# Kernel tuning notes

Measured on AMD Instinct MI355X. Metric: run time of the kernel, lower is better.

## Reference

```python
import jax, jax.numpy as jnp
import numpy as np

VOCAB, DIM, NC, KS, NCLASS = 50000, 300, 256, 3, 3
B, L1, L2 = 128, 512, 32
PAD = (KS - 1) // 2


def setup_inputs() -> dict:
    key = jax.random.key(0)
    ks = jax.random.split(key, 12)
    return {
        "context_ids": jax.random.randint(ks[0], (B, L1), 0, VOCAB),
        "context_masks": jnp.ones((B, L1), jnp.float32),
        "aspect_ids": jax.random.randint(ks[1], (B, L2), 0, VOCAB),
        "aspect_masks": jnp.ones((B, L2), jnp.float32),
        "wordmat": jax.random.normal(ks[2], (VOCAB, DIM), jnp.float32) * 0.1,
        "W": jax.random.normal(ks[3], (DIM, DIM), jnp.float32) * (2.0 / DIM) ** 0.5,
        "ctx_w": jax.random.normal(ks[4], (NC, DIM, KS), jnp.float32) * 0.02,
        "ctx_b": jnp.zeros((NC,), jnp.float32),
        "gate_w": jax.random.normal(ks[5], (NC, 2 * DIM, KS), jnp.float32) * 0.02,
        "gate_b": jnp.zeros((NC,), jnp.float32),
        "lin_w": jax.random.normal(ks[6], (NCLASS, NC), jnp.float32) * 0.05,
        "lin_b": jnp.zeros((NCLASS,), jnp.float32),
    }


def masked_softmax(A, mask):
    # A: (b, l1, l2); mask: (b, l2); normalize over dim=1 (l1), faithful to source
    A_max = jnp.max(A, axis=1, keepdims=True)
    A_exp = jnp.exp(A - A_max) * mask[:, None, :]
    return A_exp / (jnp.sum(A_exp, axis=1, keepdims=True) + 1e-10)


def conv1d(x, w, b):
    # x: (B, C_in, L), w: (C_out, C_in, K) -> (B, C_out, L)
    y = jax.lax.conv_general_dilated(x, w, (1,), [(PAD, PAD)],
                                     dimension_numbers=("NCH", "OIH", "NCH"))
    return y + b[None, :, None]


def reference(context_ids, context_masks, aspect_ids, aspect_masks,
              wordmat, W, ctx_w, ctx_b, gate_w, gate_b, lin_w, lin_b):
    context = wordmat[context_ids]          # (B, L1, D)
    aspect = wordmat[aspect_ids]            # (B, L2, D)
    # FullyAwareAttention
    sx = jax.nn.relu(jnp.einsum("bld,de->ble", context, W))
    sy = jax.nn.relu(jnp.einsum("bld,de->ble", aspect, W))
    s = jnp.einsum("bie,bje->bij", sx, sy)  # (B, L1, L2)
    alpha = masked_softmax(s, aspect_masks)
    att = jnp.einsum("bij,bjd->bid", alpha, aspect)  # (B, L1, D)
    gate_input = jnp.concatenate([context, att], axis=-1)  # (B, L1, 2D)
    sentiment = jnp.tanh(conv1d(context.transpose(0, 2, 1), ctx_w, ctx_b))
    gate = jax.nn.relu(conv1d(gate_input.transpose(0, 2, 1), gate_w, gate_b))
    out = jnp.max(sentiment * gate, axis=2)  # global maxpool over length
    return out @ lin_w.T + lin_b
```

## Files before the change

kernel.cpp:

```cpp
#include <hip/hip_runtime.h>
#include <hip/hip_bf16.h>
#include <math.h>
#include <stdint.h>

#define DIM 300
#define NC 256
#define KS 3
#define NCLASS 3
#define BB 128
#define L1 512
#define L2 32

#define XW 352
#define XROWS 514
#define ROW_B (XW * 2)
#define NKC 11
#define WP2_ELEMS (2 * 4 * 10 * 3 * 4 * 64 * 8)
#define WB_ELEMS (10 * 19 * 64 * 8)
#define WG2_ELEMS (3 * 10 * 16 * 64 * 8)
#define GT_ELEMS (BB * 3 * 32 * 256)
#define GATH_ELEMS (BB * L2 * 320)
#define WAVE_WP_B (10 * 3 * 4 * 1024)

#define ABUF_B 4224
#define EP_LD 516

typedef __attribute__((ext_vector_type(8))) short bf16x8;
typedef __attribute__((ext_vector_type(4))) short bf16x4;
typedef __attribute__((ext_vector_type(4))) float f32x4;

#define GLOBAL_AS __attribute__((address_space(1)))
#define LDS_AS __attribute__((address_space(3)))

__device__ __forceinline__ void gload_lds16(const void* g, void* l) {
    __builtin_amdgcn_global_load_lds((const GLOBAL_AS void*)g, (LDS_AS void*)l, 16, 0, 0);
}

static __device__ __forceinline__ short bfr(float x) {
    __hip_bfloat16 h = __float2bfloat16(x);
    return *(short*)&h;
}

__global__ void prep_all(const float* __restrict__ ctx_w,
                         const float* __restrict__ gate_w,
                         const float* __restrict__ Wm,
                         const int* __restrict__ aids,
                         const float* __restrict__ wordmat,
                         __hip_bfloat16* __restrict__ Wp2,
                         __hip_bfloat16* __restrict__ Wb,
                         __hip_bfloat16* __restrict__ Wg2,
                         __hip_bfloat16* __restrict__ aspb,
                         __hip_bfloat16* __restrict__ syb) {
    int idx = blockIdx.x * 256 + threadIdx.x;
    if (idx < WP2_ELEMS) {
        int jj = idx & 7;
        int lane = (idx >> 3) & 63;
        int n = (idx >> 9) & 3;
        int rest = idx >> 11;
        int tap = rest % 3;
        int r2 = rest / 3;
        int kc = r2 % 10;
        int w = r2 / 10;
        int role = w & 3, cbv = w >> 2;
        int k = kc * 32 + ((lane >> 4) << 3) + jj;
        int nl = role * 64 + n * 16 + (lane & 15);
        float v = 0.f;
        if (nl < 128) {
            int ch = cbv * 128 + nl;
            if (k < 300) v = ctx_w[(ch * DIM + k) * KS + tap];
        } else {
            int ch = cbv * 128 + (nl - 128);
            if (k < 300) v = gate_w[(ch * 2 * DIM + k) * KS + tap];
        }
        Wp2[idx] = __float2bfloat16(v);
        return;
    }
    idx -= WP2_ELEMS;
    if (idx < WB_ELEMS) {
        int j = idx & 7;
        int l = (idx >> 3) & 63;
        int r = idx >> 9;
        int nf = r % 19, kc = r / 19;
        int k = kc * 32 + ((l >> 4) << 3) + j;
        int n = nf * 16 + (l & 15);
        float v = (k < 300 && n < 300) ? Wm[k * DIM + n] : 0.f;
        Wb[idx] = __float2bfloat16(v);
        return;
    }
    idx -= WB_ELEMS;
    if (idx < WG2_ELEMS) {
        int jj = idx & 7;
        int lane = (idx >> 3) & 63;
        int rest = idx >> 9;
        int nf = rest % 16;
        int r2 = rest / 16;
        int kc = r2 % 10, tap = r2 / 10;
        int k = kc * 32 + ((lane >> 4) << 3) + jj;
        int n = nf * 16 + (lane & 15);
        float v = (k < 300) ? gate_w[(n * 2 * DIM + DIM + k) * KS + tap] : 0.f;
        Wg2[idx] = __float2bfloat16(v);
        return;
    }
    idx -= WG2_ELEMS;
    if (idx < GATH_ELEMS) {
        int row = idx / 320, d = idx - row * 320;
        if (d < DIM) {
            aspb[(size_t)row * 320 + d] = __float2bfloat16(wordmat[(size_t)aids[row] * DIM + d]);
        } else {
            aspb[(size_t)row * 320 + d] = __float2bfloat16(0.f);
            if (d >= 304) syb[(size_t)row * 320 + d] = __float2bfloat16(0.f);
        }
    }
}

__global__ __launch_bounds__(256) void xcat_x(const int* __restrict__ cids,
                                              const float* __restrict__ wordmat,
                                              __hip_bfloat16* __restrict__ Xc) {
    int t = threadIdx.x;
    int rloc = t >> 5, lane = t & 31;
    int row = blockIdx.x * 8 + rloc;
    int b = row >> 9, l = row & 511;
    size_t id = (size_t)cids[row];
    const float4* src = (const float4*)(wordmat + id * DIM);
    __hip_bfloat16* dst = Xc + ((size_t)b * XROWS + 1 + l) * XW;
    #pragma unroll
    for (int c = lane; c < 80; c += 32) {
        bf16x4 o;
        if (c < 75) {
            float4 f = src[c];
            o[0] = bfr(f.x); o[1] = bfr(f.y); o[2] = bfr(f.z); o[3] = bfr(f.w);
        } else {
            o = (bf16x4)0;
        }
        ((bf16x4*)dst)[c] = o;
    }
    if (blockIdx.x < 256 && t < 88) {
        int b2 = blockIdx.x >> 1;
        int gr = (blockIdx.x & 1) ? (XROWS - 1) : 0;
        ((bf16x4*)(Xc + ((size_t)b2 * XROWS + gr) * XW))[t] = (bf16x4)0;
    }
}

__global__ __launch_bounds__(256, 2) void asp_mfma(
        const __hip_bfloat16* __restrict__ aspb,
        const __hip_bfloat16* __restrict__ Wb,
        const __hip_bfloat16* __restrict__ Wg2,
        __hip_bfloat16* __restrict__ syb,
        __hip_bfloat16* __restrict__ Gt) {
    const int t = threadIdx.x, wave = t >> 6, l = t & 63;
    const int lane15 = l & 15, lq = l >> 4;
    if (blockIdx.x < 64) {
        const int g = blockIdx.x * 64 + wave * 16 + lane15;
        f32x4 acc[19];
        #pragma unroll
        for (int nf = 0; nf < 19; ++nf) acc[nf] = (f32x4)0.f;
        const bf16x8* Arow = (const bf16x8*)((const char*)aspb + (size_t)g * 640);
        const bf16x8* WbV = (const bf16x8*)Wb;
        for (int kc = 0; kc < 10; ++kc) {
            bf16x8 af = Arow[kc * 4 + lq];
            #pragma unroll
            for (int nf = 0; nf < 19; ++nf)
                acc[nf] = __builtin_amdgcn_mfma_f32_16x16x32_bf16(
                    af, WbV[(kc * 19 + nf) * 64 + l], acc[nf], 0, 0, 0);
        }
        #pragma unroll
        for (int nf = 0; nf < 19; ++nf) {
            int col = nf * 16 + lane15;
            #pragma unroll
            for (int i2 = 0; i2 < 4; ++i2) {
                int row = blockIdx.x * 64 + wave * 16 + lq * 4 + i2;
                syb[(size_t)row * 320 + col] = __float2bfloat16(fmaxf(acc[nf][i2], 0.f));
            }
        }
    } else {
        const int i = blockIdx.x - 64;
        const int b = i / 3, tap = i - b * 3;
        f32x4 acc[2][4];
        #pragma unroll
        for (int m = 0; m < 2; ++m)
            #pragma unroll
            for (int ni = 0; ni < 4; ++ni) acc[m][ni] = (f32x4)0.f;
        const char* Ab = (const char*)aspb + (size_t)b * 32 * 640;
        const bf16x8* WgV = (const bf16x8*)Wg2;
        for (int kc = 0; kc < 10; ++kc) {
            bf16x8 af[2];
            #pragma unroll
            for (int m = 0; m < 2; ++m)
                af[m] = *(const bf16x8*)(Ab + (size_t)(m * 16 + lane15) * 640 + kc * 64 + lq * 16);
            #pragma unroll
            for (int ni = 0; ni < 4; ++ni) {
                bf16x8 bw = WgV[((size_t)(tap * 10 + kc) * 16 + wave * 4 + ni) * 64 + l];
                #pragma unroll
                for (int m = 0; m < 2; ++m)
                    acc[m][ni] = __builtin_amdgcn_mfma_f32_16x16x32_bf16(af[m], bw, acc[m][ni], 0, 0, 0);
            }
        }
        #pragma unroll
        for (int m = 0; m < 2; ++m)
            #pragma unroll
            for (int ni = 0; ni < 4; ++ni) {
                int c = (wave * 4 + ni) * 16 + lane15;
                #pragma unroll
                for (int i2 = 0; i2 < 4; ++i2) {
                    int j = m * 16 + lq * 4 + i2;
                    Gt[((size_t)(b * 3 + tap) * 32 + j) * 256 + c] = __float2bfloat16(acc[m][ni][i2]);
                }
            }
    }
}

__global__ __launch_bounds__(256, 2) void sxs_mfma(
        const __hip_bfloat16* __restrict__ Xc,
        const __hip_bfloat16* __restrict__ Wb,
        const __hip_bfloat16* __restrict__ syb,
        float* __restrict__ s) {
    __shared__ __align__(16) char sxL[4 * 16 * 640];
    const int t = threadIdx.x, wave = t >> 6, l = t & 63;
    const int lane15 = l & 15, lq = l >> 4;
    const int lb = blockIdx.x, b = blockIdx.y;
    const int g = b * XROWS + 1 + lb * 64 + wave * 16 + lane15;

    f32x4 acc[19];
    #pragma unroll
    for (int nf = 0; nf < 19; ++nf) acc[nf] = (f32x4)0.f;

    const bf16x8* Arow = (const bf16x8*)((const char*)Xc + (size_t)g * ROW_B);
    const bf16x8* WbV = (const bf16x8*)Wb;
    for (int kc = 0; kc < 10; ++kc) {
        bf16x8 af = Arow[kc * 4 + lq];
        #pragma unroll
        for (int nf = 0; nf < 19; ++nf)
            acc[nf] = __builtin_amdgcn_mfma_f32_16x16x32_bf16(
                af, WbV[(kc * 19 + nf) * 64 + l], acc[nf], 0, 0, 0);
    }

    char* sxW = sxL + wave * (16 * 640);
    if (l < 32) {
        int row = l >> 1;
        int phys = (2 + (l & 1)) ^ ((row >> 2) & 3);
        *(f32x4*)(sxW + row * 640 + 576 + phys * 16) = (f32x4)0.f;
    }
    #pragma unroll
    for (int nf = 0; nf < 19; ++nf) {
        int col = nf * 16 + lane15;
        #pragma unroll
        for (int i2 = 0; i2 < 4; ++i2) {
            int row = lq * 4 + i2;
            int off = row * 640 + ((col >> 5) << 6) +
                      ((((col >> 3) & 3) ^ ((row >> 2) & 3)) << 4) + ((col & 7) << 1);
            *(__hip_bfloat16*)(sxW + off) = __float2bfloat16(fmaxf(acc[nf][i2], 0.f));
        }
    }
    f32x4 acc2[2];
    acc2[0] = (f32x4)0.f;
    acc2[1] = (f32x4)0.f;
    const bf16x8* syV = (const bf16x8*)syb + (size_t)b * 32 * 40;
    for (int kc = 0; kc < 10; ++kc) {
        bf16x8 af2 = *(const bf16x8*)(sxW + lane15 * 640 + kc * 64 +
                                      ((lq ^ ((lane15 >> 2) & 3)) << 4));
        #pragma unroll
        for (int nj = 0; nj < 2; ++nj) {
            bf16x8 bfj = syV[(nj * 16 + lane15) * 40 + kc * 4 + lq];
            acc2[nj] = __builtin_amdgcn_mfma_f32_16x16x32_bf16(af2, bfj, acc2[nj], 0, 0, 0);
        }
    }
    #pragma unroll
    for (int nj = 0; nj < 2; ++nj)
        #pragma unroll
        for (int i2 = 0; i2 < 4; ++i2) {
            int i = lb * 64 + wave * 16 + lq * 4 + i2;
            s[((size_t)b * L1 + i) * L2 + nj * 16 + lane15] = acc2[nj][i2];
        }
}

__global__ __launch_bounds__(256) void softmax_col(const float* __restrict__ s,
                                                   const float* __restrict__ amask,
                                                   __hip_bfloat16* __restrict__ Xc) {
    __shared__ float red[256];
    __shared__ float cmax[8], cscale[8];
    int b = blockIdx.x, jh = blockIdx.y, t = threadIdx.x;
    int jl = t & 7, j = jh * 8 + jl, ii = t >> 3;
    const float* sb = s + (size_t)b * L1 * L2;
    float v[16];
    float m = -1e30f;
    #pragma unroll
    for (int q = 0; q < 16; ++q) {
        v[q] = sb[(size_t)(ii + q * 32) * L2 + j];
        m = fmaxf(m, v[q]);
    }
    red[t] = m;
    __syncthreads();
    if (t < 8) {
        float mm = red[t];
        for (int p = 1; p < 32; ++p) mm = fmaxf(mm, red[p * 8 + t]);
        cmax[t] = mm;
    }
    __syncthreads();
    float cm = cmax[jl];
    float sum = 0.f;
    #pragma unroll
    for (int q = 0; q < 16; ++q) {
        v[q] = expf(v[q] - cm);
        sum += v[q];
    }
    red[t] = sum;
    __syncthreads();
    if (t < 8) {
        float ss = 0.f;
        for (int p = 0; p < 32; ++p) ss += red[p * 8 + t];
        float mk = amask[b * L2 + jh * 8 + t];
        cscale[t] = mk / (mk * ss + 1e-10f);
    }
    __syncthreads();
    float sc = cscale[jl];
    #pragma unroll
    for (int q = 0; q < 16; ++q) {
        int row = ii + q * 32;
        Xc[((size_t)b * XROWS + 1 + row) * XW + 320 + j] = __float2bfloat16(v[q] * sc);
    }
}

__global__ __launch_bounds__(512, 4) void conv_mfma(
        const __hip_bfloat16* __restrict__ Xc,
        const __hip_bfloat16* __restrict__ Wp2,
        const __hip_bfloat16* __restrict__ Gt,
        const float* __restrict__ ctx_b,
        const float* __restrict__ gate_b,
        float* __restrict__ part) {
    __shared__ __align__(16) char lds[16 * EP_LD * 4];
    const int t = threadIdx.x, wave = t >> 6, lane = t & 63;
    const int lane15 = lane & 15, lq = lane >> 4;
    const int lb = blockIdx.x, b = blockIdx.y, l0 = lb * 64;
    const bool isGate = wave >= 4;
    const int u = isGate ? wave - 4 : wave;
    const int cbv = u >> 1;
    const int role = isGate ? 2 + (u & 1) : (u & 1);

    f32x4 acc[4][4];
    #pragma unroll
    for (int m = 0; m < 4; ++m)
        #pragma unroll
        for (int n = 0; n < 4; ++n) acc[m][n] = (f32x4)0.f;

    const char* XcB = (const char*)Xc + ((size_t)b * XROWS + l0) * ROW_B;
    const char* bbase = (const char*)Wp2 + (size_t)(cbv * 4 + role) * WAVE_WP_B + lane * 16;

    #define STAGE_A(kc_, buf_) do {                                              \
        char* Ab_ = lds + (buf_) * ABUF_B;                                       \
        int chunk = wave * 64 + lane;                                            \
        if (chunk < 264) {                                                       \
            int row_ = chunk >> 2, c_ = chunk & 3;                               \
            int sc_ = (c_ ^ ((row_ >> 1) & 3)) << 4;                             \
            gload_lds16(XcB + (size_t)row_ * ROW_B + (kc_) * 64 + sc_,           \
                        Ab_ + wave * 1024);                                      \
        }                                                                        \
    } while (0)

    STAGE_A(0, 0);
    __syncthreads();

    for (int kc = 0; kc < NKC; ++kc) {
        const int cbuf = kc & 1;
        if (kc < NKC - 1) STAGE_A(kc + 1, cbuf ^ 1);
        const char* Ab = lds + cbuf * ABUF_B;
        if (kc < 10) {
            #pragma unroll
            for (int tap = 0; tap < 3; ++tap) {
                bf16x8 bw[4];
                #pragma unroll
                for (int n = 0; n < 4; ++n)
                    bw[n] = *(const bf16x8*)(bbase + (size_t)((kc * 3 + tap) * 4 + n) * 1024);
                bf16x8 af[4];
                #pragma unroll
                for (int m = 0; m < 4; ++m) {
                    int row = m * 16 + lane15 + tap;
                    af[m] = *(const bf16x8*)(Ab + row * 64 + ((lq ^ ((row >> 1) & 3)) << 4));
                }
                #pragma unroll
                for (int m = 0; m < 4; ++m)
                    #pragma unroll
                    for (int n = 0; n < 4; ++n)
                        acc[m][n] = __builtin_amdgcn_mfma_f32_16x16x32_bf16(
                            af[m], bw[n], acc[m][n], 0, 0, 0);
            }
        } else if (isGate) {
            const char* GtB = (const char*)Gt + (size_t)b * 3 * (32 * 256 * 2);
            #pragma unroll
            for (int tap = 0; tap < 3; ++tap) {
                bf16x8 bw[4];
                #pragma unroll
                for (int n = 0; n < 4; ++n) {
                    #pragma unroll
                    for (int jj = 0; jj < 8; ++jj)
                        ((short*)&bw[n])[jj] = *(const short*)(GtB +
                            (size_t)tap * (32 * 256 * 2) +
                            (size_t)(lq * 8 + jj) * 512 +
                            (size_t)(u * 64 + n * 16 + lane15) * 2);
                }
                bf16x8 af[4];
                #pragma unroll
                for (int m = 0; m < 4; ++m) {
                    int row = m * 16 + lane15 + tap;
                    af[m] = *(const bf16x8*)(Ab + row * 64 + ((lq ^ ((row >> 1) & 3)) << 4));
                }
                #pragma unroll
                for (int m = 0; m < 4; ++m)
                    #pragma unroll
                    for (int n = 0; n < 4; ++n)
                        acc[m][n] = __builtin_amdgcn_mfma_f32_16x16x32_bf16(
                            af[m], bw[n], acc[m][n], 0, 0, 0);
            }
        }
        __syncthreads();
    }
    #undef STAGE_A

    const int cl = t & 255, rh = t >> 8;
    const float bs = ctx_b[cl];
    const float bg = gate_b[cl];
    const int colbase = (isGate ? 256 + u * 64 : u * 64);
    float* ep = (float*)lds;
    float pm = -1e30f;
    for (int ms = 0; ms < 4; ++ms) {
        __syncthreads();
        #pragma unroll
        for (int n = 0; n < 4; ++n) {
            int col = colbase + (n << 4) + lane15;
            #pragma unroll
            for (int i2 = 0; i2 < 4; ++i2)
                ep[(lq * 4 + i2) * EP_LD + col] = acc[ms][n][i2];
        }
        __syncthreads();
        #pragma unroll
        for (int rr = 0; rr < 8; ++rr) {
            int r = rh * 8 + rr;
            float sv = ep[r * EP_LD + cl] + bs;
            float gv = ep[r * EP_LD + 256 + cl] + bg;
            pm = fmaxf(pm, tanhf(sv) * fmaxf(gv, 0.f));
        }
    }
    __syncthreads();
    ep[t] = pm;
    __syncthreads();
    if (t < 256)
        part[((size_t)b * 8 + lb) * 256 + t] = fmaxf(ep[t], ep[t + 256]);
}

__global__ __launch_bounds__(256) void finalize(const float* __restrict__ part,
                                                const float* __restrict__ lin_w,
                                                const float* __restrict__ lin_b,
                                                float* __restrict__ out) {
    __shared__ float pl[256];
    __shared__ float red[256];
    int b = blockIdx.x, t = threadIdx.x;
    float p = part[((size_t)b * 8) * 256 + t];
    for (int lb = 1; lb < 8; ++lb)
        p = fmaxf(p, part[((size_t)b * 8 + lb) * 256 + t]);
    pl[t] = p;
    __syncthreads();
    for (int n = 0; n < NCLASS; ++n) {
        red[t] = pl[t] * lin_w[n * NC + t];
        __syncthreads();
        for (int sft = 128; sft > 0; sft >>= 1) {
            if (t < sft) red[t] += red[t + sft];
            __syncthreads();
        }
        if (t == 0) out[b * NCLASS + n] = red[0] + lin_b[n];
        __syncthreads();
    }
}

extern "C" void kernel_launch(void* const* d_in, const int* in_sizes, int n_in,
                              void* d_out, int out_size, void* d_ws, size_t ws_size,
                              hipStream_t stream) {
    const int* cids = (const int*)d_in[0];
    const int* aids = (const int*)d_in[2];
    const float* amask = (const float*)d_in[3];
    const float* wordmat = (const float*)d_in[4];
    const float* Wm = (const float*)d_in[5];
    const float* ctx_w = (const float*)d_in[6];
    const float* ctx_b = (const float*)d_in[7];
    const float* gate_w = (const float*)d_in[8];
    const float* gate_b = (const float*)d_in[9];
    const float* lin_w = (const float*)d_in[10];
    const float* lin_b = (const float*)d_in[11];
    float* out = (float*)d_out;

    float* sbuf = (float*)d_ws;
    float* part = sbuf + 2097152;
    __hip_bfloat16* aspb = (__hip_bfloat16*)(part + 262144);
    __hip_bfloat16* sybf = aspb + 1310720;
    __hip_bfloat16* Wb   = sybf + 1310720;
    __hip_bfloat16* Wp2  = Wb + WB_ELEMS;
    __hip_bfloat16* Wg2  = Wp2 + WP2_ELEMS;
    __hip_bfloat16* Gt   = Wg2 + WG2_ELEMS;
    __hip_bfloat16* Xc   = Gt + GT_ELEMS;

    const int prepN = WP2_ELEMS + WB_ELEMS + WG2_ELEMS + GATH_ELEMS;
    prep_all<<<(prepN + 255) / 256, 256, 0, stream>>>(ctx_w, gate_w, Wm, aids, wordmat,
                                                      Wp2, Wb, Wg2, aspb, sybf);
    xcat_x<<<BB * L1 / 8, 256, 0, stream>>>(cids, wordmat, Xc);
    asp_mfma<<<64 + BB * 3, 256, 0, stream>>>(aspb, Wb, Wg2, sybf, Gt);
    sxs_mfma<<<dim3(L1 / 64, BB), 256, 0, stream>>>(Xc, Wb, sybf, sbuf);
    softmax_col<<<dim3(BB, 4), 256, 0, stream>>>(sbuf, amask, Xc);
    conv_mfma<<<dim3(8, BB), 512, 0, stream>>>(Xc, Wp2, Gt, ctx_b, gate_b, part);
    finalize<<<BB, 256, 0, stream>>>(part, lin_w, lin_b, out);
}
```

Measured before the change: 171.6 us.

## Double-buffer two K-chunks per barrier in conv_mfma and merge the context gather

The conv_mfma main loop now stages two K-chunks per phase into a double-buffered LDS region. The next pair's global-to-LDS loads are issued partway through the current compute, which roughly halves the number of block barriers. Separately, the context embedding gather (xcat_x) is folded into prep_all as extra blocks, removing one kernel launch. The cost is a larger LDS staging footprint and more complex phase and buffer indexing.

Measured after the change: 395.0 us. 2.3x slower.

```diff
diff --git a/kernel.cpp b/kernel.cpp
--- a/kernel.cpp
+++ b/kernel.cpp
@@ -21,6 +21,8 @@
 #define GT_ELEMS (BB * 3 * 32 * 256)
 #define GATH_ELEMS (BB * L2 * 320)
 #define WAVE_WP_B (10 * 3 * 4 * 1024)
+#define PREP_BLOCKS ((WP2_ELEMS + WB_ELEMS + WG2_ELEMS + GATH_ELEMS) / 256)
+#define XCAT_BLOCKS (BB * L1 / 8)
 
 #define ABUF_B 4224
 #define EP_LD 516
@@ -45,12 +47,41 @@
                          const float* __restrict__ gate_w,
                          const float* __restrict__ Wm,
                          const int* __restrict__ aids,
+                         const int* __restrict__ cids,
                          const float* __restrict__ wordmat,
                          __hip_bfloat16* __restrict__ Wp2,
                          __hip_bfloat16* __restrict__ Wb,
                          __hip_bfloat16* __restrict__ Wg2,
                          __hip_bfloat16* __restrict__ aspb,
-                         __hip_bfloat16* __restrict__ syb) {
+                         __hip_bfloat16* __restrict__ syb,
+                         __hip_bfloat16* __restrict__ Xc) {
+    if (blockIdx.x >= PREP_BLOCKS) {
+        int xb = blockIdx.x - PREP_BLOCKS;
+        int t = threadIdx.x;
+        int rloc = t >> 5, lane = t & 31;
+        int row = xb * 8 + rloc;
+        int b = row >> 9, l = row & 511;
+        size_t id = (size_t)cids[row];
+        const float4* src = (const float4*)(wordmat + id * DIM);
+        __hip_bfloat16* dst = Xc + ((size_t)b * XROWS + 1 + l) * XW;
+        #pragma unroll
+        for (int c = lane; c < 80; c += 32) {
+            bf16x4 o;
+            if (c < 75) {
+                float4 f = src[c];
+                o[0] = bfr(f.x); o[1] = bfr(f.y); o[2] = bfr(f.z); o[3] = bfr(f.w);
+            } else {
+                o = (bf16x4)0;
+            }
+            ((bf16x4*)dst)[c] = o;
+        }
+        if (xb < 256 && t < 88) {
+            int b2 = xb >> 1;
+            int gr = (xb & 1) ? (XROWS - 1) : 0;
+            ((bf16x4*)(Xc + ((size_t)b2 * XROWS + gr) * XW))[t] = (bf16x4)0;
+        }
+        return;
+    }
     int idx = blockIdx.x * 256 + threadIdx.x;
     if (idx < WP2_ELEMS) {
         int jj = idx & 7;
@@ -113,34 +144,6 @@
     }
 }
 
-__global__ __launch_bounds__(256) void xcat_x(const int* __restrict__ cids,
-                                              const float* __restrict__ wordmat,
-                                              __hip_bfloat16* __restrict__ Xc) {
-    int t = threadIdx.x;
-    int rloc = t >> 5, lane = t & 31;
-    int row = blockIdx.x * 8 + rloc;
-    int b = row >> 9, l = row & 511;
-    size_t id = (size_t)cids[row];
-    const float4* src = (const float4*)(wordmat + id * DIM);
-    __hip_bfloat16* dst = Xc + ((size_t)b * XROWS + 1 + l) * XW;
-    #pragma unroll
-    for (int c = lane; c < 80; c += 32) {
-        bf16x4 o;
-        if (c < 75) {
-            float4 f = src[c];
-            o[0] = bfr(f.x); o[1] = bfr(f.y); o[2] = bfr(f.z); o[3] = bfr(f.w);
-        } else {
-            o = (bf16x4)0;
-        }
-        ((bf16x4*)dst)[c] = o;
-    }
-    if (blockIdx.x < 256 && t < 88) {
-        int b2 = blockIdx.x >> 1;
-        int gr = (blockIdx.x & 1) ? (XROWS - 1) : 0;
-        ((bf16x4*)(Xc + ((size_t)b2 * XROWS + gr) * XW))[t] = (bf16x4)0;
-    }
-}
-
 __global__ __launch_bounds__(256, 2) void asp_mfma(
         const __hip_bfloat16* __restrict__ aspb,
         const __hip_bfloat16* __restrict__ Wb,
@@ -345,45 +348,61 @@
     const char* XcB = (const char*)Xc + ((size_t)b * XROWS + l0) * ROW_B;
     const char* bbase = (const char*)Wp2 + (size_t)(cbv * 4 + role) * WAVE_WP_B + lane * 16;
 
-    #define STAGE_A(kc_, buf_) do {                                              \
-        char* Ab_ = lds + (buf_) * ABUF_B;                                       \
-        int chunk = wave * 64 + lane;                                            \
-        if (chunk < 264) {                                                       \
+    #define STAGE_A(kc_, half_, pb_) do {                                        \
+        if (lane < 33) {                                                         \
+            int chunk = wave * 33 + lane;                                        \
             int row_ = chunk >> 2, c_ = chunk & 3;                               \
             int sc_ = (c_ ^ ((row_ >> 1) & 3)) << 4;                             \
             gload_lds16(XcB + (size_t)row_ * ROW_B + (kc_) * 64 + sc_,           \
-                        Ab_ + wave * 1024);                                      \
+                        lds + (pb_) * (2 * ABUF_B) + (half_) * ABUF_B + wave * 528); \
         }                                                                        \
     } while (0)
 
-    STAGE_A(0, 0);
-    __syncthreads();
-
-    for (int kc = 0; kc < NKC; ++kc) {
-        const int cbuf = kc & 1;
-        if (kc < NKC - 1) STAGE_A(kc + 1, cbuf ^ 1);
-        const char* Ab = lds + cbuf * ABUF_B;
-        if (kc < 10) {
-            #pragma unroll
-            for (int tap = 0; tap < 3; ++tap) {
-                bf16x8 bw[4];
+    STAGE_A(0, 0, 0);
+    STAGE_A(1, 1, 0);
+    __syncthreads();
+
+    #pragma unroll 1
+    for (int ph = 0; ph < 6; ++ph) {
+        const int pbuf = ph & 1;
+        const char* AbP = lds + pbuf * (2 * ABUF_B);
+        if (ph < 5) {
+            #pragma unroll
+            for (int half = 0; half < 2; ++half) {
+                const int kc = 2 * ph + half;
+                const char* Ab = AbP + half * ABUF_B;
                 #pragma unroll
-                for (int n = 0; n < 4; ++n)
-                    bw[n] = *(const bf16x8*)(bbase + (size_t)((kc * 3 + tap) * 4 + n) * 1024);
-                bf16x8 af[4];
-                #pragma unroll
-                for (int m = 0; m < 4; ++m) {
-                    int row = m * 16 + lane15 + tap;
-                    af[m] = *(const bf16x8*)(Ab + row * 64 + ((lq ^ ((row >> 1) & 3)) << 4));
-                }
-                #pragma unroll
-                for (int m = 0; m < 4; ++m)
+                for (int tap = 0; tap < 3; ++tap) {
+                    bf16x8 bw[4];
                     #pragma unroll
                     for (int n = 0; n < 4; ++n)
-                        acc[m][n] = __builtin_amdgcn_mfma_f32_16x16x32_bf16(
-                            af[m], bw[n], acc[m][n], 0, 0, 0);
+                        bw[n] = *(const bf16x8*)(bbase +
+                                (size_t)((kc * 3 + tap) * 4 + n) * 1024);
+                    if (half == 1 && tap == 2) {
+                        if (ph < 4) {
+                            STAGE_A(2 * ph + 2, 0, pbuf ^ 1);
+                            STAGE_A(2 * ph + 3, 1, pbuf ^ 1);
+                        } else {
+                            STAGE_A(10, 0, pbuf ^ 1);
+                        }
+                    }
+                    bf16x8 af[4];
+                    #pragma unroll
+                    for (int m = 0; m < 4; ++m) {
+                        int row = m * 16 + lane15 + tap;
+                        af[m] = *(const bf16x8*)(Ab + row * 64 +
+                                                 ((lq ^ ((row >> 1) & 3)) << 4));
+                    }
+                    #pragma unroll
+                    for (int m = 0; m < 4; ++m)
+                        #pragma unroll
+                        for (int n = 0; n < 4; ++n)
+                            acc[m][n] = __builtin_amdgcn_mfma_f32_16x16x32_bf16(
+                                af[m], bw[n], acc[m][n], 0, 0, 0);
+                }
             }
         } else if (isGate) {
+            const char* Ab = AbP;
             const char* GtB = (const char*)Gt + (size_t)b * 3 * (32 * 256 * 2);
             #pragma unroll
             for (int tap = 0; tap < 3; ++tap) {
@@ -401,7 +420,8 @@
                 #pragma unroll
                 for (int m = 0; m < 4; ++m) {
                     int row = m * 16 + lane15 + tap;
-                    af[m] = *(const bf16x8*)(Ab + row * 64 + ((lq ^ ((row >> 1) & 3)) << 4));
+                    af[m] = *(const bf16x8*)(Ab + row * 64 +
+                                             ((lq ^ ((row >> 1) & 3)) << 4));
                 }
                 #pragma unroll
                 for (int m = 0; m < 4; ++m)
@@ -496,10 +516,8 @@
     __hip_bfloat16* Gt   = Wg2 + WG2_ELEMS;
     __hip_bfloat16* Xc   = Gt + GT_ELEMS;
 
-    const int prepN = WP2_ELEMS + WB_ELEMS + WG2_ELEMS + GATH_ELEMS;
-    prep_all<<<(prepN + 255) / 256, 256, 0, stream>>>(ctx_w, gate_w, Wm, aids, wordmat,
-                                                      Wp2, Wb, Wg2, aspb, sybf);
-    xcat_x<<<BB * L1 / 8, 256, 0, stream>>>(cids, wordmat, Xc);
+    prep_all<<<PREP_BLOCKS + XCAT_BLOCKS, 256, 0, stream>>>(
+        ctx_w, gate_w, Wm, aids, cids, wordmat, Wp2, Wb, Wg2, aspb, sybf, Xc);
     asp_mfma<<<64 + BB * 3, 256, 0, stream>>>(aspb, Wb, Wg2, sybf, Gt);
     sxs_mfma<<<dim3(L1 / 64, BB), 256, 0, stream>>>(Xc, Wb, sybf, sbuf);
     softmax_col<<<dim3(BB, 4), 256, 0, stream>>>(sbuf, amask, Xc);
```

## Split conv into two kernel variants and fuse xcat gather into prep kernel

Applied to the files above, without the earlier changes.

Merges the context-embedding gather kernel into the prep kernel as extra blocks, removing one launch. Replaces the single conv kernel with two variants, each handling half the batch. The first uses 256-thread blocks that each cover one 128-channel half. The second gives every wave its own double-buffered LDS staging and waits with vmcnt instead of block barriers. This aims to cut barrier stalls and raise occupancy, at the cost of more code and more LDS per block in the per-wave variant.

Result: slower. 396.5 us (+131.0%).

```diff
diff --git a/kernel.cpp b/kernel.cpp
--- a/kernel.cpp
+++ b/kernel.cpp
@@ -21,9 +21,12 @@
 #define GT_ELEMS (BB * 3 * 32 * 256)
 #define GATH_ELEMS (BB * L2 * 320)
 #define WAVE_WP_B (10 * 3 * 4 * 1024)
+#define PREP_BLOCKS ((WP2_ELEMS + WB_ELEMS + WG2_ELEMS + GATH_ELEMS) / 256)
+#define XCAT_BLOCKS (BB * L1 / 8)
 
 #define ABUF_B 4224
-#define EP_LD 516
+#define EP_LD1 260
+#define EP_LD2 516
 
 typedef __attribute__((ext_vector_type(8))) short bf16x8;
 typedef __attribute__((ext_vector_type(4))) short bf16x4;
@@ -45,12 +48,41 @@
                          const float* __restrict__ gate_w,
                          const float* __restrict__ Wm,
                          const int* __restrict__ aids,
+                         const int* __restrict__ cids,
                          const float* __restrict__ wordmat,
                          __hip_bfloat16* __restrict__ Wp2,
                          __hip_bfloat16* __restrict__ Wb,
                          __hip_bfloat16* __restrict__ Wg2,
                          __hip_bfloat16* __restrict__ aspb,
-                         __hip_bfloat16* __restrict__ syb) {
+                         __hip_bfloat16* __restrict__ syb,
+                         __hip_bfloat16* __restrict__ Xc) {
+    if (blockIdx.x >= PREP_BLOCKS) {
+        int xb = blockIdx.x - PREP_BLOCKS;
+        int t = threadIdx.x;
+        int rloc = t >> 5, lane = t & 31;
+        int row = xb * 8 + rloc;
+        int b = row >> 9, l = row & 511;
+        size_t id = (size_t)cids[row];
+        const float4* src = (const float4*)(wordmat + id * DIM);
+        __hip_bfloat16* dst = Xc + ((size_t)b * XROWS + 1 + l) * XW;
+        #pragma unroll
+        for (int c = lane; c < 80; c += 32) {
+            bf16x4 o;
+            if (c < 75) {
+                float4 f = src[c];
+                o[0] = bfr(f.x); o[1] = bfr(f.y); o[2] = bfr(f.z); o[3] = bfr(f.w);
+            } else {
+                o = (bf16x4)0;
+            }
+            ((bf16x4*)dst)[c] = o;
+        }
+        if (xb < 256 && t < 88) {
+            int b2 = xb >> 1;
+            int gr = (xb & 1) ? (XROWS - 1) : 0;
+            ((bf16x4*)(Xc + ((size_t)b2 * XROWS + gr) * XW))[t] = (bf16x4)0;
+        }
+        return;
+    }
     int idx = blockIdx.x * 256 + threadIdx.x;
     if (idx < WP2_ELEMS) {
         int jj = idx & 7;
@@ -113,34 +145,6 @@
     }
 }
 
-__global__ __launch_bounds__(256) void xcat_x(const int* __restrict__ cids,
-                                              const float* __restrict__ wordmat,
-                                              __hip_bfloat16* __restrict__ Xc) {
-    int t = threadIdx.x;
-    int rloc = t >> 5, lane = t & 31;
-    int row = blockIdx.x * 8 + rloc;
-    int b = row >> 9, l = row & 511;
-    size_t id = (size_t)cids[row];
-    const float4* src = (const float4*)(wordmat + id * DIM);
-    __hip_bfloat16* dst = Xc + ((size_t)b * XROWS + 1 + l) * XW;
-    #pragma unroll
-    for (int c = lane; c < 80; c += 32) {
-        bf16x4 o;
-        if (c < 75) {
-            float4 f = src[c];
-            o[0] = bfr(f.x); o[1] = bfr(f.y); o[2] = bfr(f.z); o[3] = bfr(f.w);
-        } else {
-            o = (bf16x4)0;
-        }
-        ((bf16x4*)dst)[c] = o;
-    }
-    if (blockIdx.x < 256 && t < 88) {
-        int b2 = blockIdx.x >> 1;
-        int gr = (blockIdx.x & 1) ? (XROWS - 1) : 0;
-        ((bf16x4*)(Xc + ((size_t)b2 * XROWS + gr) * XW))[t] = (bf16x4)0;
-    }
-}
-
 __global__ __launch_bounds__(256, 2) void asp_mfma(
         const __hip_bfloat16* __restrict__ aspb,
         const __hip_bfloat16* __restrict__ Wb,
@@ -320,21 +324,19 @@
     }
 }
 
-__global__ __launch_bounds__(512, 4) void conv_mfma(
+__global__ __launch_bounds__(256, 4) void conv_v7(
         const __hip_bfloat16* __restrict__ Xc,
         const __hip_bfloat16* __restrict__ Wp2,
         const __hip_bfloat16* __restrict__ Gt,
         const float* __restrict__ ctx_b,
         const float* __restrict__ gate_b,
         float* __restrict__ part) {
-    __shared__ __align__(16) char lds[16 * EP_LD * 4];
+    __shared__ __align__(16) char lds[16 * EP_LD1 * 4];
     const int t = threadIdx.x, wave = t >> 6, lane = t & 63;
     const int lane15 = lane & 15, lq = lane >> 4;
-    const int lb = blockIdx.x, b = blockIdx.y, l0 = lb * 64;
-    const bool isGate = wave >= 4;
-    const int u = isGate ? wave - 4 : wave;
-    const int cbv = u >> 1;
-    const int role = isGate ? 2 + (u & 1) : (u & 1);
+    const int lb = blockIdx.x >> 1, cb = blockIdx.x & 1;
+    const int b = blockIdx.y, l0 = lb * 64;
+    const int role = wave ^ ((blockIdx.x & 1) << 1);
 
     f32x4 acc[4][4];
     #pragma unroll
@@ -343,16 +345,19 @@
         for (int n = 0; n < 4; ++n) acc[m][n] = (f32x4)0.f;
 
     const char* XcB = (const char*)Xc + ((size_t)b * XROWS + l0) * ROW_B;
-    const char* bbase = (const char*)Wp2 + (size_t)(cbv * 4 + role) * WAVE_WP_B + lane * 16;
+    const char* bbase = (const char*)Wp2 + (size_t)(cb * 4 + role) * WAVE_WP_B + lane * 16;
 
     #define STAGE_A(kc_, buf_) do {                                              \
         char* Ab_ = lds + (buf_) * ABUF_B;                                       \
-        int chunk = wave * 64 + lane;                                            \
-        if (chunk < 264) {                                                       \
-            int row_ = chunk >> 2, c_ = chunk & 3;                               \
-            int sc_ = (c_ ^ ((row_ >> 1) & 3)) << 4;                             \
-            gload_lds16(XcB + (size_t)row_ * ROW_B + (kc_) * 64 + sc_,           \
-                        Ab_ + wave * 1024);                                      \
+        _Pragma("unroll")                                                        \
+        for (int i = 0; i < 2; ++i) {                                            \
+            int chunk = (i * 4 + wave) * 64 + lane;                              \
+            if (chunk < 264) {                                                   \
+                int row_ = chunk >> 2, c_ = chunk & 3;                           \
+                int sc_ = (c_ ^ ((row_ >> 1) & 3)) << 4;                         \
+                gload_lds16(XcB + (size_t)row_ * ROW_B + (kc_) * 64 + sc_,       \
+                            Ab_ + (i * 4 + wave) * 1024);                        \
+            }                                                                    \
         }                                                                        \
     } while (0)
 
@@ -370,6 +375,136 @@
                 #pragma unroll
                 for (int n = 0; n < 4; ++n)
                     bw[n] = *(const bf16x8*)(bbase + (size_t)((kc * 3 + tap) * 4 + n) * 1024);
+                bf16x8 af[4];
+                #pragma unroll
+                for (int m = 0; m < 4; ++m) {
+                    int row = m * 16 + lane15 + tap;
+                    af[m] = *(const bf16x8*)(Ab + row * 64 + ((lq ^ ((row >> 1) & 3)) << 4));
+                }
+                #pragma unroll
+                for (int m = 0; m < 4; ++m)
+                    #pragma unroll
+                    for (int n = 0; n < 4; ++n)
+                        acc[m][n] = __builtin_amdgcn_mfma_f32_16x16x32_bf16(
+                            af[m], bw[n], acc[m][n], 0, 0, 0);
+            }
+        } else if (role >= 2) {
+            const char* GtB = (const char*)Gt + (size_t)b * 3 * (32 * 256 * 2);
+            #pragma unroll
+            for (int tap = 0; tap < 3; ++tap) {
+                bf16x8 bw[4];
+                #pragma unroll
+                for (int n = 0; n < 4; ++n) {
+                    #pragma unroll
+                    for (int jj = 0; jj < 8; ++jj)
+                        ((short*)&bw[n])[jj] = *(const short*)(GtB +
+                            (size_t)tap * (32 * 256 * 2) +
+                            (size_t)(lq * 8 + jj) * 512 +
+                            (size_t)(cb * 128 + (role & 1) * 64 + n * 16 + lane15) * 2);
+                }
+                bf16x8 af[4];
+                #pragma unroll
+                for (int m = 0; m < 4; ++m) {
+                    int row = m * 16 + lane15 + tap;
+                    af[m] = *(const bf16x8*)(Ab + row * 64 + ((lq ^ ((row >> 1) & 3)) << 4));
+                }
+                #pragma unroll
+                for (int m = 0; m < 4; ++m)
+                    #pragma unroll
+                    for (int n = 0; n < 4; ++n)
+                        acc[m][n] = __builtin_amdgcn_mfma_f32_16x16x32_bf16(
+                            af[m], bw[n], acc[m][n], 0, 0, 0);
+            }
+        }
+        __syncthreads();
+    }
+    #undef STAGE_A
+
+    const int c0 = cb * 128;
+    const int cl = t & 127, rh = t >> 7;
+    const float bs = ctx_b[c0 + cl];
+    const float bg = gate_b[c0 + cl];
+    float* ep = (float*)lds;
+    float pm = -1e30f;
+    for (int ms = 0; ms < 4; ++ms) {
+        __syncthreads();
+        #pragma unroll
+        for (int n = 0; n < 4; ++n) {
+            int col = (role << 6) + (n << 4) + lane15;
+            #pragma unroll
+            for (int i2 = 0; i2 < 4; ++i2)
+                ep[(lq * 4 + i2) * EP_LD1 + col] = acc[ms][n][i2];
+        }
+        __syncthreads();
+        #pragma unroll
+        for (int rr = 0; rr < 8; ++rr) {
+            int r = rh * 8 + rr;
+            float sv = ep[r * EP_LD1 + cl] + bs;
+            float gv = ep[r * EP_LD1 + 128 + cl] + bg;
+            pm = fmaxf(pm, tanhf(sv) * fmaxf(gv, 0.f));
+        }
+    }
+    __syncthreads();
+    ep[t] = pm;
+    __syncthreads();
+    if (t < 128)
+        part[((size_t)b * 8 + lb) * 256 + c0 + cl] = fmaxf(ep[t], ep[t + 128]);
+}
+
+__global__ __launch_bounds__(512, 4) void conv_pw(
+        const __hip_bfloat16* __restrict__ Xc,
+        const __hip_bfloat16* __restrict__ Wp2,
+        const __hip_bfloat16* __restrict__ Gt,
+        const float* __restrict__ ctx_b,
+        const float* __restrict__ gate_b,
+        float* __restrict__ part) {
+    __shared__ __align__(16) char lds[8 * 2 * ABUF_B];
+    const int t = threadIdx.x, wave = t >> 6, lane = t & 63;
+    const int lane15 = lane & 15, lq = lane >> 4;
+    const int lb = blockIdx.x, b = blockIdx.y + 64, l0 = lb * 64;
+    const bool isGate = wave >= 4;
+    const int u = isGate ? wave - 4 : wave;
+    const int cbv = u >> 1;
+    const int role = isGate ? 2 + (u & 1) : (u & 1);
+
+    f32x4 acc[4][4];
+    #pragma unroll
+    for (int m = 0; m < 4; ++m)
+        #pragma unroll
+        for (int n = 0; n < 4; ++n) acc[m][n] = (f32x4)0.f;
+
+    const char* XcB = (const char*)Xc + ((size_t)b * XROWS + l0) * ROW_B;
+    const char* bbase = (const char*)Wp2 + (size_t)(cbv * 4 + role) * WAVE_WP_B + lane * 16;
+    char* myB = lds + wave * (2 * ABUF_B);
+
+    #define STG(kc_, buf_) do {                                                  \
+        _Pragma("unroll")                                                        \
+        for (int i_ = 0; i_ < 5; ++i_) {                                         \
+            int chunk = i_ * 64 + lane;                                          \
+            if (chunk < 264) {                                                   \
+                int row_ = chunk >> 2, c_ = chunk & 3;                           \
+                int sc_ = (c_ ^ ((row_ >> 1) & 3)) << 4;                         \
+                gload_lds16(XcB + (size_t)row_ * ROW_B + (kc_) * 64 + sc_,       \
+                            myB + (buf_) * ABUF_B + i_ * 1024);                  \
+            }                                                                    \
+        }                                                                        \
+    } while (0)
+
+    STG(0, 0);
+
+    #pragma unroll 1
+    for (int kc = 0; kc < NKC; ++kc) {
+        const int cbuf = kc & 1;
+        asm volatile("s_waitcnt vmcnt(0)" ::: "memory");
+        const char* Ab = myB + cbuf * ABUF_B;
+        if (kc < 10) {
+            #pragma unroll
+            for (int tap = 0; tap < 3; ++tap) {
+                bf16x8 bw[4];
+                #pragma unroll
+                for (int n = 0; n < 4; ++n)
+                    bw[n] = *(const bf16x8*)(bbase + (size_t)((kc * 3 + tap) * 4 + n) * 1024);
+                if (tap == 2) STG(kc + 1, cbuf ^ 1);
                 bf16x8 af[4];
                 #pragma unroll
                 for (int m = 0; m < 4; ++m) {
@@ -411,9 +546,8 @@
                             af[m], bw[n], acc[m][n], 0, 0, 0);
             }
         }
-        __syncthreads();
-    }
-    #undef STAGE_A
+    }
+    #undef STG
 
     const int cl = t & 255, rh = t >> 8;
     const float bs = ctx_b[cl];
@@ -428,14 +562,14 @@
             int col = colbase + (n << 4) + lane15;
             #pragma unroll
             for (int i2 = 0; i2 < 4; ++i2)
-                ep[(lq * 4 + i2) * EP_LD + col] = acc[ms][n][i2];
+                ep[(lq * 4 + i2) * EP_LD2 + col] = acc[ms][n][i2];
         }
         __syncthreads();
         #pragma unroll
         for (int rr = 0; rr < 8; ++rr) {
             int r = rh * 8 + rr;
-            float sv = ep[r * EP_LD + cl] + bs;
-            float gv = ep[r * EP_LD + 256 + cl] + bg;
+            float sv = ep[r * EP_LD2 + cl] + bs;
+            float gv = ep[r * EP_LD2 + 256 + cl] + bg;
             pm = fmaxf(pm, tanhf(sv) * fmaxf(gv, 0.f));
         }
     }
@@ -496,13 +630,12 @@
     __hip_bfloat16* Gt   = Wg2 + WG2_ELEMS;
     __hip_bfloat16* Xc   = Gt + GT_ELEMS;
 
-    const int prepN = WP2_ELEMS + WB_ELEMS + WG2_ELEMS + GATH_ELEMS;
-    prep_all<<<(prepN + 255) / 256, 256, 0, stream>>>(ctx_w, gate_w, Wm, aids, wordmat,
-                                                      Wp2, Wb, Wg2, aspb, sybf);
-    xcat_x<<<BB * L1 / 8, 256, 0, stream>>>(cids, wordmat, Xc);
+    prep_all<<<PREP_BLOCKS + XCAT_BLOCKS, 256, 0, stream>>>(
+        ctx_w, gate_w, Wm, aids, cids, wordmat, Wp2, Wb, Wg2, aspb, sybf, Xc);
     asp_mfma<<<64 + BB * 3, 256, 0, stream>>>(aspb, Wb, Wg2, sybf, Gt);
     sxs_mfma<<<dim3(L1 / 64, BB), 256, 0, stream>>>(Xc, Wb, sybf, sbuf);
     softmax_col<<<dim3(BB, 4), 256, 0, stream>>>(sbuf, amask, Xc);
-    conv_mfma<<<dim3(8, BB), 512, 0, stream>>>(Xc, Wp2, Gt, ctx_b, gate_b, part);
+    conv_v7<<<dim3(16, 64), 256, 0, stream>>>(Xc, Wp2, Gt, ctx_b, gate_b, part);
+    conv_pw<<<dim3(8, 64), 512, 0, stream>>>(Xc, Wp2, Gt, ctx_b, gate_b, part);
     finalize<<<BB, 256, 0, stream>>>(part, lin_w, lin_b, out);
 }
```
